# Performance work log

Measured on AMD Instinct MI355X. Metric: run time of the kernel, lower is better.

## Reference

```python
import jax, jax.numpy as jnp
import numpy as np

B, N, C, H = 8, 1024, 768, 12
HEAD_DIM = C // H
EPS = 1e-6


def setup_inputs() -> dict:
    key = jax.random.key(0)
    k1, k2, k3, k4, k5 = jax.random.split(key, 5)
    x = jax.random.normal(k1, (B, N, C), dtype=jnp.float32)
    # binary keep-mask per token, shape (B, N, 1)
    policy = (jax.random.uniform(k2, (B, N, 1)) > 0.3).astype(jnp.float32)
    Wqkv = jax.random.normal(k3, (3 * C, C), dtype=jnp.float32) * 0.02
    Wproj = jax.random.normal(k4, (C, C), dtype=jnp.float32) * 0.02
    bproj = jax.random.normal(k5, (C,), dtype=jnp.float32) * 0.02
    return {"x": x, "policy": policy, "Wqkv": Wqkv, "Wproj": Wproj, "bproj": bproj}


def softmax_with_policy(attn, policy, eps=EPS):
    # attn: (B,H,N,N), policy: (B,N,1) in {0,1}
    Bb, _, Nn, _ = attn.shape
    ap1 = policy.reshape(Bb, 1, 1, Nn)          # key mask
    ap2 = policy.reshape(Bb, 1, Nn, 1)          # query mask
    eye = jnp.eye(Nn, dtype=policy.dtype)[None, None]
    attn_policy = ap1 * ap2 + (1.0 - ap1) * eye  # (B,1,N,N)
    max_att = jnp.max(attn, axis=-1, keepdims=True)
    a = jnp.exp(attn - max_att).astype(jnp.float32) * attn_policy.astype(jnp.float32)
    a = (a + eps / Nn) / (jnp.sum(a, axis=-1, keepdims=True) + eps)
    return a.astype(attn.dtype)


def reference(x, policy, Wqkv, Wproj, bproj):
    Bb, Nn, Cc = x.shape
    scale = HEAD_DIM ** -0.5
    qkv = (x @ Wqkv.T).reshape(Bb, Nn, 3, H, HEAD_DIM).transpose(2, 0, 3, 1, 4)
    q, k, v = qkv[0], qkv[1], qkv[2]            # each (B,H,N,hd)
    attn = jnp.einsum('bhnd,bhmd->bhnm', q, k) * scale
    attn = softmax_with_policy(attn, policy)
    out = jnp.einsum('bhnm,bhmd->bhnd', attn, v)  # (B,H,N,hd)
    out = out.transpose(0, 2, 1, 3).reshape(Bb, Nn, Cc)
    return out @ Wproj.T + bproj
```

## Files before the change

kernel.cpp:

```cpp
#include <hip/hip_runtime.h>
#include <hip/hip_bf16.h>
#include <stdint.h>

#define Bdim 8
#define Nseq 1024
#define Cdim 768
#define Hn 12
#define HD 64
#define EPSf 1e-6f

typedef __bf16 bf16;
typedef __bf16 bf16x8 __attribute__((ext_vector_type(8)));
typedef float f32x4 __attribute__((ext_vector_type(4)));

static __device__ __forceinline__ void gload_lds16(const bf16* g, bf16* lds) {
  __builtin_amdgcn_global_load_lds(
      (const __attribute__((address_space(1))) uint32_t*)g,
      (__attribute__((address_space(3))) uint32_t*)lds, 16, 0, 0);
}

#define NX (Bdim * Nseq * Cdim)
#define NWQ (3 * Cdim * Cdim)
#define NWP (Cdim * Cdim)
__global__ __launch_bounds__(256) void cvt_all(
    const float* __restrict__ x, const float* __restrict__ wq, const float* __restrict__ wp,
    bf16* __restrict__ Xb, bf16* __restrict__ Wqb, bf16* __restrict__ Wpb,
    float* __restrict__ CS) {
  if (blockIdx.x < 24) CS[blockIdx.x * 256 + threadIdx.x] = 0.f;
  const int i = (blockIdx.x * 256 + threadIdx.x) * 8;
  const float* src;
  bf16* dst;
  int off;
  if (i < NX) { src = x; dst = Xb; off = i; }
  else if (i < NX + NWQ) { src = wq; dst = Wqb; off = i - NX; }
  else { src = wp; dst = Wpb; off = i - NX - NWQ; }
  float4 a = *(const float4*)(src + off);
  float4 b = *(const float4*)(src + off + 4);
  bf16x8 o;
  o[0] = (bf16)a.x; o[1] = (bf16)a.y; o[2] = (bf16)a.z; o[3] = (bf16)a.w;
  o[4] = (bf16)b.x; o[5] = (bf16)b.y; o[6] = (bf16)b.z; o[7] = (bf16)b.w;
  *(bf16x8*)(dst + off) = o;
}

__global__ __launch_bounds__(256) void gemm_qkv(
    const bf16* __restrict__ X, const bf16* __restrict__ W,
    bf16* __restrict__ Qb, bf16* __restrict__ Kb, bf16* __restrict__ Vt,
    float* __restrict__ CS) {
  __shared__ __align__(16) bf16 As[128 * 64];
  __shared__ __align__(16) bf16 Bs[128 * 64];
  const int t = threadIdx.x;
  const int lane = t & 63;
  const int w = t >> 6;
  const int l15 = lane & 15, quad = lane >> 4;
  const int wm = w & 1, wn = w >> 1;
  constexpr int K = Cdim;

  const int flat = blockIdx.y * 18 + blockIdx.x;
  const int xcd = flat & 7, idx = flat >> 3;
  const int my = (idx & 7) + xcd * 8;
  const int nx = idx >> 3;
  const int mbase = my * 128;
  const int nbase = nx * 128;

  const int srow = t >> 3, slot = t & 7;
  f32x4 acc[4][4] = {};

  for (int kt = 0; kt < K; kt += 64) {
#pragma unroll
    for (int j = 0; j < 4; j++) {
      const int row = j * 32 + srow;
      const int seg = slot ^ (row & 7);
      gload_lds16(X + (size_t)(mbase + row) * K + kt + seg * 8, As + (j * 256 + t) * 8);
    }
#pragma unroll
    for (int j = 0; j < 4; j++) {
      const int row = j * 32 + srow;
      const int seg = slot ^ (row & 7);
      gload_lds16(W + (size_t)(nbase + row) * K + kt + seg * 8, Bs + (j * 256 + t) * 8);
    }
    __syncthreads();
#pragma unroll
    for (int kh = 0; kh < 2; kh++) {
      bf16x8 a[4], b[4];
#pragma unroll
      for (int mt = 0; mt < 4; mt++) {
        const int row = wm * 64 + mt * 16 + l15;
        a[mt] = *(const bf16x8*)(As + row * 64 + ((kh * 4 + quad) ^ (row & 7)) * 8);
      }
#pragma unroll
      for (int nt = 0; nt < 4; nt++) {
        const int row = wn * 64 + nt * 16 + l15;
        b[nt] = *(const bf16x8*)(Bs + row * 64 + ((kh * 4 + quad) ^ (row & 7)) * 8);
      }
#pragma unroll
      for (int mt = 0; mt < 4; mt++)
#pragma unroll
        for (int nt = 0; nt < 4; nt++)
          acc[mt][nt] = __builtin_amdgcn_mfma_f32_16x16x32_bf16(a[mt], b[nt], acc[mt][nt], 0, 0, 0);
    }
    __syncthreads();
  }

  const int s = nbase / Cdim;
  const float oscale = (s == 0) ? 0.125f : 1.0f;
  const int jbase = (nbase % Cdim) + wn * 64;
  const int b0 = mbase >> 10;
#pragma unroll
  for (int nt = 0; nt < 4; nt++) {
    const int jj = jbase + nt * 16 + l15;
    const int h = jj >> 6, d = jj & 63;
#pragma unroll
    for (int mt = 0; mt < 4; mt++) {
#pragma unroll
      for (int r = 0; r < 4; r++) {
        const int m = mbase + wm * 64 + mt * 16 + quad * 4 + r;
        const int n = m & 1023;
        const bf16 v = (bf16)(acc[mt][nt][r] * oscale);
        const size_t bh = (size_t)b0 * Hn + h;
        if (s == 0)      Qb[(bh * Nseq + n) * HD + d] = v;
        else if (s == 1) Kb[(bh * Nseq + n) * HD + d] = v;
        else             Vt[(bh * HD + d) * Nseq + n] = v;
      }
    }
  }
  if (s == 2) {
#pragma unroll
    for (int nt = 0; nt < 4; nt++) {
      float v = 0.f;
#pragma unroll
      for (int mt = 0; mt < 4; mt++)
#pragma unroll
        for (int r = 0; r < 4; r++) v += acc[mt][nt][r];
      v += __shfl_xor(v, 16);
      v += __shfl_xor(v, 32);
      if (quad == 0) {
        const int jj = jbase + nt * 16 + l15;
        atomicAdd(&CS[((size_t)b0 * Hn + (jj >> 6)) * HD + (jj & 63)], v);
      }
    }
  }
}

template <bool DIAG>
static __device__ __forceinline__ void smax_update(
    f32x4 (&S)[2][4], float (&mx)[2][4], float (&lrow)[2][4],
    const float (&polq)[2][4], const float (&polk)[4],
    int kt, int qbase, int quad, int l15) {
#pragma unroll
  for (int u = 0; u < 2; u++)
#pragma unroll
    for (int r = 0; r < 4; r++) {
      const float pm = polq[u][r];
      const float m4 = fmaxf(fmaxf(S[u][0][r], S[u][1][r]), fmaxf(S[u][2][r], S[u][3][r]));
      mx[u][r] = fmaxf(mx[u][r], m4);
      const int q = qbase + u * 16 + quad * 4 + r;
      float psum = 0.f;
#pragma unroll
      for (int s = 0; s < 4; s++) {
        const float e = __expf(S[u][s][r]);
        float p = e * (polk[s] * pm);
        if (DIAG) p = (q == kt + s * 16 + l15) ? e : p;
        S[u][s][r] = p;
        psum += p;
      }
      lrow[u][r] += psum;
    }
}

__global__ __launch_bounds__(256) void attn_fused(
    const bf16* __restrict__ Qb, const bf16* __restrict__ Kb, const bf16* __restrict__ Vt,
    const float* __restrict__ pol, const float* __restrict__ CS, bf16* __restrict__ O) {
  __shared__ __align__(16) bf16 Ks[64 * 64];
  __shared__ __align__(16) bf16 Vs[64 * 64];
  __shared__ __align__(16) bf16 Pbuf[4][32 * 40];
  __shared__ float Ps[Nseq];
  const int t = threadIdx.x, w = t >> 6, lane = t & 63;
  const int l15 = lane & 15, quad = lane >> 4;

  const int bx = blockIdx.x;
  const int g = (bx & 7) + 8 * (bx >> 6);
  const int qt = (bx >> 3) & 7;
  const int b_ = g / Hn, h = g % Hn;
  const int qbase = qt * 128 + w * 32;
  const int ktdiag = qbase & ~63;

  const bf16* Qp = Qb + (size_t)g * Nseq * HD;
  const bf16* Kp = Kb + (size_t)g * Nseq * HD;
  const bf16* Vp = Vt + (size_t)g * HD * Nseq;
  const float* polb = pol + (size_t)b_ * Nseq;

  *(float4*)(Ps + t * 4) = *(const float4*)(polb + t * 4);

  const int ci0 = t, ci1 = t + 256;
  const int row0 = ci0 >> 3, seg0 = (ci0 & 7) ^ (row0 & 7);
  const int row1 = ci1 >> 3, seg1 = (ci1 & 7) ^ (row1 & 7);

  bf16x8 aq[2][2];
#pragma unroll
  for (int u = 0; u < 2; u++) {
    aq[u][0] = *(const bf16x8*)(Qp + (qbase + u * 16 + l15) * HD + quad * 8);
    aq[u][1] = *(const bf16x8*)(Qp + (qbase + u * 16 + l15) * HD + 32 + quad * 8);
  }

  float polq[2][4];
#pragma unroll
  for (int u = 0; u < 2; u++)
#pragma unroll
    for (int r = 0; r < 4; r++) polq[u][r] = polb[qbase + u * 16 + quad * 4 + r];

  float mx[2][4], lrow[2][4];
  f32x4 oacc[2][4] = {};
#pragma unroll
  for (int u = 0; u < 2; u++)
#pragma unroll
    for (int r = 0; r < 4; r++) { mx[u][r] = -1e30f; lrow[u][r] = 0.f; }

  bf16* Pw = &Pbuf[w][0];
  const int swA = (quad ^ (l15 & 7)) * 8;
  const int swB = ((quad ^ 4) ^ (l15 & 7)) * 8;

  for (int kt = 0; kt < Nseq; kt += 64) {
    __syncthreads();
    gload_lds16(Kp + (kt + row0) * HD + seg0 * 8, Ks + ci0 * 8);
    gload_lds16(Kp + (kt + row1) * HD + seg1 * 8, Ks + ci1 * 8);
    gload_lds16(Vp + (size_t)row0 * Nseq + kt + seg0 * 8, Vs + ci0 * 8);
    gload_lds16(Vp + (size_t)row1 * Nseq + kt + seg1 * 8, Vs + ci1 * 8);
    __syncthreads();

    f32x4 S[2][4] = {};
#pragma unroll
    for (int s = 0; s < 4; s++) {
      const int i = s * 16 + l15;
      bf16x8 bk0 = *(const bf16x8*)(Ks + i * 64 + swA);
      bf16x8 bk1 = *(const bf16x8*)(Ks + i * 64 + swB);
#pragma unroll
      for (int u = 0; u < 2; u++) {
        S[u][s] = __builtin_amdgcn_mfma_f32_16x16x32_bf16(aq[u][0], bk0, S[u][s], 0, 0, 0);
        S[u][s] = __builtin_amdgcn_mfma_f32_16x16x32_bf16(aq[u][1], bk1, S[u][s], 0, 0, 0);
      }
    }

    float polk[4];
#pragma unroll
    for (int s = 0; s < 4; s++) polk[s] = Ps[kt + s * 16 + l15];

    if (kt == ktdiag)
      smax_update<true>(S, mx, lrow, polq, polk, kt, qbase, quad, l15);
    else
      smax_update<false>(S, mx, lrow, polq, polk, kt, qbase, quad, l15);

#pragma unroll
    for (int hh = 0; hh < 2; hh++) {
#pragma unroll
      for (int u = 0; u < 2; u++)
#pragma unroll
        for (int sl = 0; sl < 2; sl++)
#pragma unroll
          for (int r = 0; r < 4; r++)
            Pw[(u * 16 + quad * 4 + r) * 40 + sl * 16 + l15] = (bf16)S[u][hh * 2 + sl][r];
      asm volatile("s_waitcnt lgkmcnt(0)" ::: "memory");
      bf16x8 ap[2];
#pragma unroll
      for (int u = 0; u < 2; u++)
        ap[u] = *(const bf16x8*)(Pw + (u * 16 + l15) * 40 + quad * 8);
      const int swV = (((hh * 4 + quad)) ^ (l15 & 7)) * 8;
#pragma unroll
      for (int c = 0; c < 4; c++) {
        const int i = c * 16 + l15;
        bf16x8 bv = *(const bf16x8*)(Vs + i * 64 + swV);
#pragma unroll
        for (int u = 0; u < 2; u++)
          oacc[u][c] = __builtin_amdgcn_mfma_f32_16x16x32_bf16(ap[u], bv, oacc[u][c], 0, 0, 0);
      }
    }
  }

  float rden[2][4], eterm[2][4];
  const float epsN = EPSf / (float)Nseq;
#pragma unroll
  for (int u = 0; u < 2; u++)
#pragma unroll
    for (int r = 0; r < 4; r++) {
      float v = lrow[u][r];
      v += __shfl_xor(v, 1);
      v += __shfl_xor(v, 2);
      v += __shfl_xor(v, 4);
      v += __shfl_xor(v, 8);
      float m = mx[u][r];
      m = fmaxf(m, __shfl_xor(m, 1));
      m = fmaxf(m, __shfl_xor(m, 2));
      m = fmaxf(m, __shfl_xor(m, 4));
      m = fmaxf(m, __shfl_xor(m, 8));
      const float em = __expf(m);
      rden[u][r] = 1.f / (v + EPSf * em);
      eterm[u][r] = epsN * em;
    }
  const float* CSp = CS + (size_t)g * HD;
#pragma unroll
  for (int c = 0; c < 4; c++) {
    const float cs = CSp[c * 16 + l15];
#pragma unroll
    for (int u = 0; u < 2; u++)
#pragma unroll
      for (int r = 0; r < 4; r++) {
        const int q = qbase + u * 16 + quad * 4 + r;
        const float val = (oacc[u][c][r] + cs * eterm[u][r]) * rden[u][r];
        O[((size_t)b_ * Nseq + q) * Cdim + h * 64 + c * 16 + l15] = (bf16)val;
      }
  }
}

__global__ __launch_bounds__(256) void gemm_proj(
    const bf16* __restrict__ A_, const bf16* __restrict__ W,
    const float* __restrict__ bias, float* __restrict__ out) {
  __shared__ __align__(16) bf16 As[64 * 64];
  __shared__ __align__(16) bf16 Bs[128 * 64];
  const int t = threadIdx.x;
  const int lane = t & 63;
  const int wn = t >> 6;
  const int l15 = lane & 15, quad = lane >> 4;
  constexpr int K = Cdim;

  const int flat = blockIdx.y * 6 + blockIdx.x;
  const int xcd = flat & 7, idx = flat >> 3;
  const int my = (idx & 15) + xcd * 16;
  const int nx = idx >> 4;
  const int mbase = my * 64;
  const int nbase = nx * 128;

  const int srow = t >> 3, slot = t & 7;
  f32x4 acc[4][2] = {};

  for (int kt = 0; kt < K; kt += 64) {
#pragma unroll
    for (int j = 0; j < 2; j++) {
      const int row = j * 32 + srow;
      const int seg = slot ^ (row & 7);
      gload_lds16(A_ + (size_t)(mbase + row) * K + kt + seg * 8, As + (j * 256 + t) * 8);
    }
#pragma unroll
    for (int j = 0; j < 4; j++) {
      const int row = j * 32 + srow;
      const int seg = slot ^ (row & 7);
      gload_lds16(W + (size_t)(nbase + row) * K + kt + seg * 8, Bs + (j * 256 + t) * 8);
    }
    __syncthreads();
#pragma unroll
    for (int kh = 0; kh < 2; kh++) {
      bf16x8 a[4], b[2];
#pragma unroll
      for (int mt = 0; mt < 4; mt++) {
        const int row = mt * 16 + l15;
        a[mt] = *(const bf16x8*)(As + row * 64 + ((kh * 4 + quad) ^ (row & 7)) * 8);
      }
#pragma unroll
      for (int nt = 0; nt < 2; nt++) {
        const int row = wn * 32 + nt * 16 + l15;
        b[nt] = *(const bf16x8*)(Bs + row * 64 + ((kh * 4 + quad) ^ (row & 7)) * 8);
      }
#pragma unroll
      for (int mt = 0; mt < 4; mt++)
#pragma unroll
        for (int nt = 0; nt < 2; nt++)
          acc[mt][nt] = __builtin_amdgcn_mfma_f32_16x16x32_bf16(a[mt], b[nt], acc[mt][nt], 0, 0, 0);
    }
    __syncthreads();
  }

#pragma unroll
  for (int nt = 0; nt < 2; nt++) {
    const int j = nbase + wn * 32 + nt * 16 + l15;
    const float bj = bias[j];
#pragma unroll
    for (int mt = 0; mt < 4; mt++)
#pragma unroll
      for (int r = 0; r < 4; r++) {
        const int m = mbase + mt * 16 + quad * 4 + r;
        out[(size_t)m * Cdim + j] = acc[mt][nt][r] + bj;
      }
  }
}

extern "C" void kernel_launch(void* const* d_in, const int* in_sizes, int n_in,
                              void* d_out, int out_size, void* d_ws, size_t ws_size,
                              hipStream_t stream) {
  const float* x = (const float*)d_in[0];
  const float* pol = (const float*)d_in[1];
  const float* Wqkv = (const float*)d_in[2];
  const float* Wproj = (const float*)d_in[3];
  const float* bproj = (const float*)d_in[4];
  float* out = (float*)d_out;
  char* ws = (char*)d_ws;

  const size_t SZ = (size_t)Bdim * Hn * Nseq * HD * sizeof(bf16);
  bf16* Qb = (bf16*)(ws);
  bf16* Kb = (bf16*)(ws + SZ);
  bf16* Vt = (bf16*)(ws + 2 * SZ);
  bf16* O  = (bf16*)(ws + 3 * SZ);
  float* CS = (float*)(ws + 4 * SZ);
  bf16* Xb = (bf16*)(ws + 4 * SZ + 32 * 1024);
  bf16* Wqkvb = Xb + (size_t)Bdim * Nseq * Cdim;
  bf16* Wprojb = Wqkvb + (size_t)3 * Cdim * Cdim;

  cvt_all<<<(NX + NWQ + NWP) / 2048, 256, 0, stream>>>(x, Wqkv, Wproj, Xb, Wqkvb, Wprojb, CS);
  gemm_qkv<<<dim3(18, 64), 256, 0, stream>>>(Xb, Wqkvb, Qb, Kb, Vt, CS);
  attn_fused<<<Bdim * Hn * (Nseq / 128), 256, 0, stream>>>(Qb, Kb, Vt, pol, CS, O);
  gemm_proj<<<dim3(6, 128), 256, 0, stream>>>(O, Wprojb, bproj, out);
}
```

Before: 221.8 us.

## Keep P in registers via transposed QK^T and double-buffer K/V tiles

```diff
diff --git a/kernel.cpp b/kernel.cpp
--- a/kernel.cpp
+++ b/kernel.cpp
@@ -119,7 +119,10 @@
         const size_t bh = (size_t)b0 * Hn + h;
         if (s == 0)      Qb[(bh * Nseq + n) * HD + d] = v;
         else if (s == 1) Kb[(bh * Nseq + n) * HD + d] = v;
-        else             Vt[(bh * HD + d) * Nseq + n] = v;
+        else {
+          const int nperm = (n & ~31) | (quad * 8 + (mt & 1) * 4 + r);
+          Vt[(bh * HD + d) * Nseq + nperm] = v;
+        }
       }
     }
   }
@@ -143,36 +146,40 @@
 
 template <bool DIAG>
 static __device__ __forceinline__ void smax_update(
-    f32x4 (&S)[2][4], float (&mx)[2][4], float (&lrow)[2][4],
-    const float (&polq)[2][4], const float (&polk)[4],
+    f32x4 (&S)[2][4], float (&mx)[2], float (&lrow)[2],
+    const float (&polq)[2], const float4 (&pk)[4],
     int kt, int qbase, int quad, int l15) {
 #pragma unroll
-  for (int u = 0; u < 2; u++)
-#pragma unroll
-    for (int r = 0; r < 4; r++) {
-      const float pm = polq[u][r];
-      const float m4 = fmaxf(fmaxf(S[u][0][r], S[u][1][r]), fmaxf(S[u][2][r], S[u][3][r]));
-      mx[u][r] = fmaxf(mx[u][r], m4);
-      const int q = qbase + u * 16 + quad * 4 + r;
-      float psum = 0.f;
-#pragma unroll
-      for (int s = 0; s < 4; s++) {
-        const float e = __expf(S[u][s][r]);
-        float p = e * (polk[s] * pm);
-        if (DIAG) p = (q == kt + s * 16 + l15) ? e : p;
-        S[u][s][r] = p;
+  for (int u = 0; u < 2; u++) {
+    const float pm = polq[u];
+    const int q = qbase + u * 16 + l15;
+    float m4 = -1e30f, psum = 0.f;
+#pragma unroll
+    for (int kg = 0; kg < 4; kg++)
+#pragma unroll
+      for (int r = 0; r < 4; r++) m4 = fmaxf(m4, S[u][kg][r]);
+    mx[u] = fmaxf(mx[u], m4);
+#pragma unroll
+    for (int kg = 0; kg < 4; kg++) {
+      const float* pkk = (const float*)&pk[kg];
+#pragma unroll
+      for (int r = 0; r < 4; r++) {
+        const float e = __expf(S[u][kg][r]);
+        float p = e * (pkk[r] * pm);
+        if (DIAG) p = (q == kt + kg * 16 + quad * 4 + r) ? e : p;
+        S[u][kg][r] = p;
         psum += p;
       }
-      lrow[u][r] += psum;
-    }
+    }
+    lrow[u] += psum;
+  }
 }
 
 __global__ __launch_bounds__(256) void attn_fused(
     const bf16* __restrict__ Qb, const bf16* __restrict__ Kb, const bf16* __restrict__ Vt,
     const float* __restrict__ pol, const float* __restrict__ CS, bf16* __restrict__ O) {
-  __shared__ __align__(16) bf16 Ks[64 * 64];
-  __shared__ __align__(16) bf16 Vs[64 * 64];
-  __shared__ __align__(16) bf16 Pbuf[4][32 * 40];
+  __shared__ __align__(16) bf16 Ks[2][64 * 64];
+  __shared__ __align__(16) bf16 Vs[2][64 * 64];
   __shared__ float Ps[Nseq];
   const int t = threadIdx.x, w = t >> 6, lane = t & 63;
   const int l15 = lane & 15, quad = lane >> 4;
@@ -201,73 +208,64 @@
     aq[u][0] = *(const bf16x8*)(Qp + (qbase + u * 16 + l15) * HD + quad * 8);
     aq[u][1] = *(const bf16x8*)(Qp + (qbase + u * 16 + l15) * HD + 32 + quad * 8);
   }
-
-  float polq[2][4];
-#pragma unroll
-  for (int u = 0; u < 2; u++)
-#pragma unroll
-    for (int r = 0; r < 4; r++) polq[u][r] = polb[qbase + u * 16 + quad * 4 + r];
-
-  float mx[2][4], lrow[2][4];
+  float polq[2] = { polb[qbase + l15], polb[qbase + 16 + l15] };
+
+  float mx[2] = { -1e30f, -1e30f }, lrow[2] = { 0.f, 0.f };
   f32x4 oacc[2][4] = {};
-#pragma unroll
-  for (int u = 0; u < 2; u++)
-#pragma unroll
-    for (int r = 0; r < 4; r++) { mx[u][r] = -1e30f; lrow[u][r] = 0.f; }
-
-  bf16* Pw = &Pbuf[w][0];
-  const int swA = (quad ^ (l15 & 7)) * 8;
-  const int swB = ((quad ^ 4) ^ (l15 & 7)) * 8;
+
+  gload_lds16(Kp + row0 * HD + seg0 * 8, &Ks[0][ci0 * 8]);
+  gload_lds16(Kp + row1 * HD + seg1 * 8, &Ks[0][ci1 * 8]);
+  gload_lds16(Vp + (size_t)row0 * Nseq + seg0 * 8, &Vs[0][ci0 * 8]);
+  gload_lds16(Vp + (size_t)row1 * Nseq + seg1 * 8, &Vs[0][ci1 * 8]);
 
   for (int kt = 0; kt < Nseq; kt += 64) {
+    const int buf = (kt >> 6) & 1;
     __syncthreads();
-    gload_lds16(Kp + (kt + row0) * HD + seg0 * 8, Ks + ci0 * 8);
-    gload_lds16(Kp + (kt + row1) * HD + seg1 * 8, Ks + ci1 * 8);
-    gload_lds16(Vp + (size_t)row0 * Nseq + kt + seg0 * 8, Vs + ci0 * 8);
-    gload_lds16(Vp + (size_t)row1 * Nseq + kt + seg1 * 8, Vs + ci1 * 8);
-    __syncthreads();
+    if (kt + 64 < Nseq) {
+      const int nb = buf ^ 1;
+      gload_lds16(Kp + (kt + 64 + row0) * HD + seg0 * 8, &Ks[nb][ci0 * 8]);
+      gload_lds16(Kp + (kt + 64 + row1) * HD + seg1 * 8, &Ks[nb][ci1 * 8]);
+      gload_lds16(Vp + (size_t)row0 * Nseq + kt + 64 + seg0 * 8, &Vs[nb][ci0 * 8]);
+      gload_lds16(Vp + (size_t)row1 * Nseq + kt + 64 + seg1 * 8, &Vs[nb][ci1 * 8]);
+    }
 
     f32x4 S[2][4] = {};
 #pragma unroll
-    for (int s = 0; s < 4; s++) {
-      const int i = s * 16 + l15;
-      bf16x8 bk0 = *(const bf16x8*)(Ks + i * 64 + swA);
-      bf16x8 bk1 = *(const bf16x8*)(Ks + i * 64 + swB);
+    for (int kg = 0; kg < 4; kg++) {
+      const int row = kg * 16 + l15;
+      bf16x8 bk0 = *(const bf16x8*)(&Ks[buf][row * 64 + ((quad ^ (row & 7)) * 8)]);
+      bf16x8 bk1 = *(const bf16x8*)(&Ks[buf][row * 64 + (((quad ^ 4) ^ (row & 7)) * 8)]);
 #pragma unroll
       for (int u = 0; u < 2; u++) {
-        S[u][s] = __builtin_amdgcn_mfma_f32_16x16x32_bf16(aq[u][0], bk0, S[u][s], 0, 0, 0);
-        S[u][s] = __builtin_amdgcn_mfma_f32_16x16x32_bf16(aq[u][1], bk1, S[u][s], 0, 0, 0);
-      }
-    }
-
-    float polk[4];
-#pragma unroll
-    for (int s = 0; s < 4; s++) polk[s] = Ps[kt + s * 16 + l15];
+        S[u][kg] = __builtin_amdgcn_mfma_f32_16x16x32_bf16(bk0, aq[u][0], S[u][kg], 0, 0, 0);
+        S[u][kg] = __builtin_amdgcn_mfma_f32_16x16x32_bf16(bk1, aq[u][1], S[u][kg], 0, 0, 0);
+      }
+    }
+
+    float4 pk[4];
+#pragma unroll
+    for (int kg = 0; kg < 4; kg++)
+      pk[kg] = *(const float4*)(Ps + kt + kg * 16 + quad * 4);
 
     if (kt == ktdiag)
-      smax_update<true>(S, mx, lrow, polq, polk, kt, qbase, quad, l15);
+      smax_update<true>(S, mx, lrow, polq, pk, kt, qbase, quad, l15);
     else
-      smax_update<false>(S, mx, lrow, polq, polk, kt, qbase, quad, l15);
+      smax_update<false>(S, mx, lrow, polq, pk, kt, qbase, quad, l15);
 
 #pragma unroll
     for (int hh = 0; hh < 2; hh++) {
+      bf16x8 ap[2];
 #pragma unroll
       for (int u = 0; u < 2; u++)
 #pragma unroll
-        for (int sl = 0; sl < 2; sl++)
-#pragma unroll
-          for (int r = 0; r < 4; r++)
-            Pw[(u * 16 + quad * 4 + r) * 40 + sl * 16 + l15] = (bf16)S[u][hh * 2 + sl][r];
-      asm volatile("s_waitcnt lgkmcnt(0)" ::: "memory");
-      bf16x8 ap[2];
-#pragma unroll
-      for (int u = 0; u < 2; u++)
-        ap[u] = *(const bf16x8*)(Pw + (u * 16 + l15) * 40 + quad * 8);
-      const int swV = (((hh * 4 + quad)) ^ (l15 & 7)) * 8;
+        for (int j = 0; j < 4; j++) {
+          ap[u][j] = (bf16)S[u][2 * hh][j];
+          ap[u][4 + j] = (bf16)S[u][2 * hh + 1][j];
+        }
 #pragma unroll
       for (int c = 0; c < 4; c++) {
-        const int i = c * 16 + l15;
-        bf16x8 bv = *(const bf16x8*)(Vs + i * 64 + swV);
+        const int row = c * 16 + l15;
+        bf16x8 bv = *(const bf16x8*)(&Vs[buf][row * 64 + (((hh * 4 + quad) ^ (row & 7)) * 8)]);
 #pragma unroll
         for (int u = 0; u < 2; u++)
           oacc[u][c] = __builtin_amdgcn_mfma_f32_16x16x32_bf16(ap[u], bv, oacc[u][c], 0, 0, 0);
@@ -275,26 +273,26 @@
     }
   }
 
+  const float epsN = EPSf / (float)Nseq;
   float rden[2][4], eterm[2][4];
-  const float epsN = EPSf / (float)Nseq;
-#pragma unroll
-  for (int u = 0; u < 2; u++)
+#pragma unroll
+  for (int u = 0; u < 2; u++) {
+    float v = lrow[u];
+    v += __shfl_xor(v, 16);
+    v += __shfl_xor(v, 32);
+    float m = mx[u];
+    m = fmaxf(m, __shfl_xor(m, 16));
+    m = fmaxf(m, __shfl_xor(m, 32));
+    const float em = __expf(m);
+    const float den = v + EPSf * em;
+    const float eN = epsN * em;
+    const int base = lane & 48;
 #pragma unroll
     for (int r = 0; r < 4; r++) {
-      float v = lrow[u][r];
-      v += __shfl_xor(v, 1);
-      v += __shfl_xor(v, 2);
-      v += __shfl_xor(v, 4);
-      v += __shfl_xor(v, 8);
-      float m = mx[u][r];
-      m = fmaxf(m, __shfl_xor(m, 1));
-      m = fmaxf(m, __shfl_xor(m, 2));
-      m = fmaxf(m, __shfl_xor(m, 4));
-      m = fmaxf(m, __shfl_xor(m, 8));
-      const float em = __expf(m);
-      rden[u][r] = 1.f / (v + EPSf * em);
-      eterm[u][r] = epsN * em;
-    }
+      rden[u][r] = 1.f / __shfl(den, base | (quad * 4 + r));
+      eterm[u][r] = __shfl(eN, base | (quad * 4 + r));
+    }
+  }
   const float* CSp = CS + (size_t)g * HD;
 #pragma unroll
   for (int c = 0; c < 4; c++) {
```

Measured after the change: 212.5 us. 1.04x faster.
